# Kernel tuning notes

Hardware: AMD Instinct MI355X
Metric: run time of the kernel (lower is better)

## Reference

```python
import jax, jax.numpy as jnp
import numpy as np

N, E, D = 40000, 640000, 128  # n_nodes, n_edges, hidden_dim
EPS = 1e-5  # equinox RMSNorm default eps


def setup_inputs() -> dict:
    key = jax.random.key(0)
    k1, k2, k3, k4 = jax.random.split(key, 4)
    x = jax.random.normal(k1, (N, D), dtype=jnp.float32)
    e = jax.random.randint(k2, (E, 2), 0, N)  # [E,2] int, col0=src, col1=dst
    W = jax.random.normal(k3, (D, D), dtype=jnp.float32) / np.sqrt(D).astype(np.float32)
    b = jax.random.normal(k4, (D,), dtype=jnp.float32) * 0.01
    g = jnp.ones((D,), dtype=jnp.float32)   # RMSNorm weight
    rb = jnp.zeros((D,), dtype=jnp.float32)  # RMSNorm bias
    return {"x": x, "e": e, "W": W, "b": b, "g": g, "rb": rb}


def reference(x, e, W, b, g, rb):
    src, dst = e[:, 0], e[:, 1]
    # gather source nodes, per-edge linear + relu  -> [E, D]
    m = jax.nn.relu(x[src] @ W.T + b)
    n = x.shape[0]
    # degree (any column of segment_sum(ones_like(m)) is the scalar degree)
    deg = jax.ops.segment_sum(jnp.ones((e.shape[0],), x.dtype), dst, num_segments=n)
    # max-aggregate messages to destination nodes  -> [N, D]
    agg = jax.ops.segment_max(m, dst, num_segments=n)
    agg = jnp.where(deg[:, None] == 0, jnp.zeros((), x.dtype), agg)
    # residual + RMSNorm
    h = x + agg
    inv = jax.lax.rsqrt(jnp.mean(h * h, axis=-1, keepdims=True) + EPS)
    return h * inv * g + rb
```

## Files before the change

### kernel.cpp

```cpp
#include <hip/hip_runtime.h>
#include <hip/hip_bf16.h>

#define D 128
#define EPS 1e-5f

typedef __bf16 bf16x8 __attribute__((ext_vector_type(8)));
typedef float  f32x4  __attribute__((ext_vector_type(4)));

__global__ __launch_bounds__(256) void gemm_relu_mfma_kernel(
    const float* __restrict__ x, const float* __restrict__ W,
    const float* __restrict__ b, float* __restrict__ y, int n)
{
    __shared__ __attribute__((aligned(16))) __bf16 Wl[128][136];
    __shared__ __attribute__((aligned(16))) __bf16 xl[64][136];

    const int tid = threadIdx.x;
    const int block_row = blockIdx.x * 64;

    for (int i = tid; i < 4096; i += 256) {
        int r = i >> 5, q = i & 31;
        float4 v = ((const float4*)W)[i];
        __bf16* p = &Wl[r][q * 4];
        p[0] = (__bf16)v.x; p[1] = (__bf16)v.y;
        p[2] = (__bf16)v.z; p[3] = (__bf16)v.w;
    }
    for (int i = tid; i < 2048; i += 256) {
        int r = i >> 5, q = i & 31;
        int gr = block_row + r;
        float4 v = make_float4(0.f, 0.f, 0.f, 0.f);
        if (gr < n) v = ((const float4*)x)[(size_t)gr * 32 + q];
        __bf16* p = &xl[r][q * 4];
        p[0] = (__bf16)v.x; p[1] = (__bf16)v.y;
        p[2] = (__bf16)v.z; p[3] = (__bf16)v.w;
    }
    __syncthreads();

    const int w  = tid >> 6;
    const int l  = tid & 63;
    const int lr = l & 15;
    const int lk = l >> 4;

    bf16x8 a[4];
#pragma unroll
    for (int ks = 0; ks < 4; ks++)
        a[ks] = *(const bf16x8*)&xl[w * 16 + lr][ks * 32 + lk * 8];

#pragma unroll
    for (int ct = 0; ct < 8; ct++) {
        f32x4 acc = {0.f, 0.f, 0.f, 0.f};
#pragma unroll
        for (int ks = 0; ks < 4; ks++) {
            bf16x8 bf = *(const bf16x8*)&Wl[ct * 16 + lr][ks * 32 + lk * 8];
            acc = __builtin_amdgcn_mfma_f32_16x16x32_bf16(a[ks], bf, acc, 0, 0, 0);
        }
        int col = ct * 16 + lr;
        float bias = b[col];
#pragma unroll
        for (int reg = 0; reg < 4; reg++) {
            int gr = block_row + w * 16 + lk * 4 + reg;
            if (gr < n)
                y[(size_t)gr * D + col] = fmaxf(acc[reg] + bias, 0.f);
        }
    }
}

__global__ __launch_bounds__(256) void hist_kernel(
    const int* __restrict__ e, int* __restrict__ counts, int E)
{
    int i = blockIdx.x * 256 + threadIdx.x;
    if (i < E) {
        int dst = e[2 * i + 1];
        atomicAdd(&counts[dst], 1);
    }
}

__global__ __launch_bounds__(256) void scan_partial_kernel(
    const int* __restrict__ counts, int* __restrict__ row_start,
    int* __restrict__ partials, int n)
{
    __shared__ int s[256];
    const int tid = threadIdx.x;
    const int i = blockIdx.x * 256 + tid;
    int v = (i < n) ? counts[i] : 0;
    s[tid] = v;
    __syncthreads();
    for (int off = 1; off < 256; off <<= 1) {
        int add = (tid >= off) ? s[tid - off] : 0;
        __syncthreads();
        s[tid] += add;
        __syncthreads();
    }
    if (i < n) row_start[i] = s[tid] - v;
    if (tid == 255) partials[blockIdx.x] = s[255];
}

__global__ __launch_bounds__(256) void scan_top_kernel(
    int* __restrict__ partials, int nb)
{
    __shared__ int s[256];
    const int tid = threadIdx.x;
    int v = (tid < nb) ? partials[tid] : 0;
    s[tid] = v;
    __syncthreads();
    for (int off = 1; off < 256; off <<= 1) {
        int add = (tid >= off) ? s[tid - off] : 0;
        __syncthreads();
        s[tid] += add;
        __syncthreads();
    }
    if (tid < nb) partials[tid] = s[tid] - v;
}

__global__ __launch_bounds__(256) void scan_add_kernel(
    int* __restrict__ row_start, const int* __restrict__ partials,
    int* __restrict__ cursor, int n)
{
    int i = blockIdx.x * 256 + threadIdx.x;
    if (i < n) {
        int v = row_start[i] + partials[blockIdx.x];
        row_start[i] = v;
        cursor[i]    = v;
    }
}

__global__ __launch_bounds__(256) void place_kernel(
    const int* __restrict__ e, int* __restrict__ cursor,
    int* __restrict__ sorted_src, int E)
{
    int i = blockIdx.x * 256 + threadIdx.x;
    if (i < E) {
        int2 ed = ((const int2*)e)[i];
        int pos = atomicAdd(&cursor[ed.y], 1);
        sorted_src[pos] = ed.x;
    }
}

__global__ __launch_bounds__(256) void seg_max_finalize_kernel(
    const int* __restrict__ row_start, const int* __restrict__ counts,
    const int* __restrict__ sorted_src, const float* __restrict__ y,
    const float* __restrict__ x, const float* __restrict__ g,
    const float* __restrict__ rb, float* __restrict__ out, int n)
{
    int row  = blockIdx.x * 4 + (threadIdx.x >> 6);
    int lane = threadIdx.x & 63;
    if (row >= n) return;

    const int start = row_start[row];
    const int cnt   = counts[row];

    float2 m = make_float2(0.f, 0.f);
    int k = 0;
    for (; k + 1 < cnt; k += 2) {
        int s0 = sorted_src[start + k];
        int s1 = sorted_src[start + k + 1];
        float2 v0 = ((const float2*)(y + (size_t)s0 * D))[lane];
        float2 v1 = ((const float2*)(y + (size_t)s1 * D))[lane];
        m.x = fmaxf(m.x, fmaxf(v0.x, v1.x));
        m.y = fmaxf(m.y, fmaxf(v0.y, v1.y));
    }
    if (k < cnt) {
        int s0 = sorted_src[start + k];
        float2 v0 = ((const float2*)(y + (size_t)s0 * D))[lane];
        m.x = fmaxf(m.x, v0.x);
        m.y = fmaxf(m.y, v0.y);
    }

    float2 xv = ((const float2*)(x + (size_t)row * D))[lane];
    float2 h  = make_float2(xv.x + m.x, xv.y + m.y);

    float ss = h.x * h.x + h.y * h.y;
#pragma unroll
    for (int off = 1; off < 64; off <<= 1) ss += __shfl_xor(ss, off);

    float inv = rsqrtf(ss * (1.0f / (float)D) + EPS);

    float2 gv = ((const float2*)g)[lane];
    float2 rv = ((const float2*)rb)[lane];
    float2 o  = make_float2(h.x * inv * gv.x + rv.x,
                            h.y * inv * gv.y + rv.y);
    ((float2*)(out + (size_t)row * D))[lane] = o;
}

extern "C" void kernel_launch(void* const* d_in, const int* in_sizes, int n_in,
                              void* d_out, int out_size, void* d_ws, size_t ws_size,
                              hipStream_t stream)
{
    const float* x  = (const float*)d_in[0];
    const int*   e  = (const int*)  d_in[1];
    const float* W  = (const float*)d_in[2];
    const float* b  = (const float*)d_in[3];
    const float* g  = (const float*)d_in[4];
    const float* rb = (const float*)d_in[5];
    float* out = (float*)d_out;

    const int n = in_sizes[0] / D;
    const int E = in_sizes[1] / 2;

    char* ws = (char*)d_ws;
    float* y         = (float*)(ws);
    int*   counts    = (int*)  (ws + 20480000);
    int*   row_start = (int*)  (ws + 20640000);
    int*   cursor    = (int*)  (ws + 20800000);
    int*   sorted_src= (int*)  (ws + 20960000);
    int*   partials  = (int*)  (ws + 23520000);

    const int nb = (n + 255) / 256;

    hipMemsetAsync(counts, 0, (size_t)n * sizeof(int), stream);

    gemm_relu_mfma_kernel<<<(n + 63) / 64, 256, 0, stream>>>(x, W, b, y, n);

    hist_kernel<<<(E + 255) / 256, 256, 0, stream>>>(e, counts, E);
    scan_partial_kernel<<<nb, 256, 0, stream>>>(counts, row_start, partials, n);
    scan_top_kernel<<<1, 256, 0, stream>>>(partials, nb);
    scan_add_kernel<<<nb, 256, 0, stream>>>(row_start, partials, cursor, n);
    place_kernel<<<(E + 255) / 256, 256, 0, stream>>>(e, cursor, sorted_src, E);

    seg_max_finalize_kernel<<<(n + 3) / 4, 256, 0, stream>>>(
        row_start, counts, sorted_src, y, x, g, rb, out, n);
}
```

Before: 217.2 us.

## Store messages in bf16, fuse histogram into GEMM, merge scan kernels

The per-node linear+ReLU output is now written as bf16 instead of fp32. This halves the bytes the segment-max kernel gathers per edge, and that kernel now unrolls the gather by four. The degree histogram is folded into the GEMM kernel with a fixed four-iteration grid-stride loop. The top-level scan is recomputed redundantly inside each scan_add block, removing a separate launch. The costs are lower message precision, and the histogram only covers all edges when E is at most four times the GEMM grid's thread count.

```diff
diff --git a/kernel.cpp b/kernel.cpp
--- a/kernel.cpp
+++ b/kernel.cpp
@@ -7,9 +7,11 @@
 typedef __bf16 bf16x8 __attribute__((ext_vector_type(8)));
 typedef float  f32x4  __attribute__((ext_vector_type(4)));
 
-__global__ __launch_bounds__(256) void gemm_relu_mfma_kernel(
+__global__ __launch_bounds__(256) void gemm_relu_hist_kernel(
     const float* __restrict__ x, const float* __restrict__ W,
-    const float* __restrict__ b, float* __restrict__ y, int n)
+    const float* __restrict__ b, __bf16* __restrict__ y,
+    const int* __restrict__ e, int* __restrict__ counts,
+    int n, int E)
 {
     __shared__ __attribute__((aligned(16))) __bf16 Wl[128][136];
     __shared__ __attribute__((aligned(16))) __bf16 xl[64][136];
@@ -35,6 +37,16 @@
     }
     __syncthreads();
 
+    {
+        int base = blockIdx.x * 256 + tid;
+        int stride = gridDim.x * 256;
+#pragma unroll
+        for (int t = 0; t < 4; t++) {
+            int i = base + t * stride;
+            if (i < E) atomicAdd(&counts[e[2 * i + 1]], 1);
+        }
+    }
+
     const int w  = tid >> 6;
     const int l  = tid & 63;
     const int lr = l & 15;
@@ -59,18 +71,8 @@
         for (int reg = 0; reg < 4; reg++) {
             int gr = block_row + w * 16 + lk * 4 + reg;
             if (gr < n)
-                y[(size_t)gr * D + col] = fmaxf(acc[reg] + bias, 0.f);
+                y[(size_t)gr * D + col] = (__bf16)fmaxf(acc[reg] + bias, 0.f);
         }
-    }
-}
-
-__global__ __launch_bounds__(256) void hist_kernel(
-    const int* __restrict__ e, int* __restrict__ counts, int E)
-{
-    int i = blockIdx.x * 256 + threadIdx.x;
-    if (i < E) {
-        int dst = e[2 * i + 1];
-        atomicAdd(&counts[dst], 1);
     }
 }
 
@@ -94,8 +96,9 @@
     if (tid == 255) partials[blockIdx.x] = s[255];
 }
 
-__global__ __launch_bounds__(256) void scan_top_kernel(
-    int* __restrict__ partials, int nb)
+__global__ __launch_bounds__(256) void scan_add_kernel(
+    int* __restrict__ row_start, const int* __restrict__ partials,
+    int* __restrict__ cursor, int n, int nb)
 {
     __shared__ int s[256];
     const int tid = threadIdx.x;
@@ -108,18 +111,13 @@
         s[tid] += add;
         __syncthreads();
     }
-    if (tid < nb) partials[tid] = s[tid] - v;
-}
-
-__global__ __launch_bounds__(256) void scan_add_kernel(
-    int* __restrict__ row_start, const int* __restrict__ partials,
-    int* __restrict__ cursor, int n)
-{
-    int i = blockIdx.x * 256 + threadIdx.x;
+    int off0 = (blockIdx.x == 0) ? 0 : s[blockIdx.x - 1];
+
+    int i = blockIdx.x * 256 + tid;
     if (i < n) {
-        int v = row_start[i] + partials[blockIdx.x];
-        row_start[i] = v;
-        cursor[i]    = v;
+        int val = row_start[i] + off0;
+        row_start[i] = val;
+        cursor[i]    = val;
     }
 }
 
@@ -137,7 +135,7 @@
 
 __global__ __launch_bounds__(256) void seg_max_finalize_kernel(
     const int* __restrict__ row_start, const int* __restrict__ counts,
-    const int* __restrict__ sorted_src, const float* __restrict__ y,
+    const int* __restrict__ sorted_src, const unsigned int* __restrict__ ybu,
     const float* __restrict__ x, const float* __restrict__ g,
     const float* __restrict__ rb, float* __restrict__ out, int n)
 {
@@ -148,27 +146,38 @@
     const int start = row_start[row];
     const int cnt   = counts[row];
 
-    float2 m = make_float2(0.f, 0.f);
+    float mx = 0.f, my = 0.f;
     int k = 0;
-    for (; k + 1 < cnt; k += 2) {
+    for (; k + 3 < cnt; k += 4) {
         int s0 = sorted_src[start + k];
         int s1 = sorted_src[start + k + 1];
-        float2 v0 = ((const float2*)(y + (size_t)s0 * D))[lane];
-        float2 v1 = ((const float2*)(y + (size_t)s1 * D))[lane];
-        m.x = fmaxf(m.x, fmaxf(v0.x, v1.x));
-        m.y = fmaxf(m.y, fmaxf(v0.y, v1.y));
-    }
-    if (k < cnt) {
+        int s2 = sorted_src[start + k + 2];
+        int s3 = sorted_src[start + k + 3];
+        unsigned int u0 = ybu[(size_t)s0 * 64 + lane];
+        unsigned int u1 = ybu[(size_t)s1 * 64 + lane];
+        unsigned int u2 = ybu[(size_t)s2 * 64 + lane];
+        unsigned int u3 = ybu[(size_t)s3 * 64 + lane];
+        mx = fmaxf(mx, fmaxf(fmaxf(__uint_as_float(u0 << 16),
+                                   __uint_as_float(u1 << 16)),
+                             fmaxf(__uint_as_float(u2 << 16),
+                                   __uint_as_float(u3 << 16))));
+        my = fmaxf(my, fmaxf(fmaxf(__uint_as_float(u0 & 0xffff0000u),
+                                   __uint_as_float(u1 & 0xffff0000u)),
+                             fmaxf(__uint_as_float(u2 & 0xffff0000u),
+                                   __uint_as_float(u3 & 0xffff0000u))));
+    }
+    for (; k < cnt; k++) {
         int s0 = sorted_src[start + k];
-        float2 v0 = ((const float2*)(y + (size_t)s0 * D))[lane];
-        m.x = fmaxf(m.x, v0.x);
-        m.y = fmaxf(m.y, v0.y);
+        unsigned int u0 = ybu[(size_t)s0 * 64 + lane];
+        mx = fmaxf(mx, __uint_as_float(u0 << 16));
+        my = fmaxf(my, __uint_as_float(u0 & 0xffff0000u));
     }
 
     float2 xv = ((const float2*)(x + (size_t)row * D))[lane];
-    float2 h  = make_float2(xv.x + m.x, xv.y + m.y);
-
-    float ss = h.x * h.x + h.y * h.y;
+    float hx = xv.x + mx;
+    float hy = xv.y + my;
+
+    float ss = hx * hx + hy * hy;
 #pragma unroll
     for (int off = 1; off < 64; off <<= 1) ss += __shfl_xor(ss, off);
 
@@ -176,8 +185,8 @@
 
     float2 gv = ((const float2*)g)[lane];
     float2 rv = ((const float2*)rb)[lane];
-    float2 o  = make_float2(h.x * inv * gv.x + rv.x,
-                            h.y * inv * gv.y + rv.y);
+    float2 o  = make_float2(hx * inv * gv.x + rv.x,
+                            hy * inv * gv.y + rv.y);
     ((float2*)(out + (size_t)row * D))[lane] = o;
 }
 
@@ -197,25 +206,24 @@
     const int E = in_sizes[1] / 2;
 
     char* ws = (char*)d_ws;
-    float* y         = (float*)(ws);
-    int*   counts    = (int*)  (ws + 20480000);
-    int*   row_start = (int*)  (ws + 20640000);
-    int*   cursor    = (int*)  (ws + 20800000);
-    int*   sorted_src= (int*)  (ws + 20960000);
-    int*   partials  = (int*)  (ws + 23520000);
+    __bf16* y        = (__bf16*)(ws);
+    int*   counts    = (int*)  (ws + 10240000);
+    int*   row_start = (int*)  (ws + 10400000);
+    int*   cursor    = (int*)  (ws + 10560000);
+    int*   sorted_src= (int*)  (ws + 10720000);
+    int*   partials  = (int*)  (ws + 13280000);
 
     const int nb = (n + 255) / 256;
+    const int gblocks = (n + 63) / 64;
 
     hipMemsetAsync(counts, 0, (size_t)n * sizeof(int), stream);
 
-    gemm_relu_mfma_kernel<<<(n + 63) / 64, 256, 0, stream>>>(x, W, b, y, n);
-
-    hist_kernel<<<(E + 255) / 256, 256, 0, stream>>>(e, counts, E);
+    gemm_relu_hist_kernel<<<gblocks, 256, 0, stream>>>(x, W, b, y, e, counts, n, E);
+
     scan_partial_kernel<<<nb, 256, 0, stream>>>(counts, row_start, partials, n);
-    scan_top_kernel<<<1, 256, 0, stream>>>(partials, nb);
-    scan_add_kernel<<<nb, 256, 0, stream>>>(row_start, partials, cursor, n);
+    scan_add_kernel<<<nb, 256, 0, stream>>>(row_start, partials, cursor, n, nb);
     place_kernel<<<(E + 255) / 256, 256, 0, stream>>>(e, cursor, sorted_src, E);
 
     seg_max_finalize_kernel<<<(n + 3) / 4, 256, 0, stream>>>(
-        row_start, counts, sorted_src, y, x, g, rb, out, n);
-}
+        row_start, counts, sorted_src, (const unsigned int*)y, x, g, rb, out, n);
+}
```

After: 192.1 us. 1.13x faster.
